# Performance work log

Measured on AMD Instinct MI355X. Metric: run time of the kernel, lower is better.

## Reference

```python
import jax, jax.numpy as jnp
import numpy as np

N = 100000
E = 800000
F_IN = 64
HID = 128


def setup_inputs() -> dict:
    key = jax.random.key(0)
    ks = jax.random.split(key, 10)
    x = jax.random.normal(ks[0], (N, F_IN), dtype=jnp.float32)
    edge_index = jax.random.randint(ks[1], (2, E), 0, N, dtype=jnp.int64)
    s = 0.05
    # PyG GraphConv: lin_rel (with bias) applied to aggregated neighbors, lin_root (no bias) to self
    return {
        "x": x,
        "edge_index": edge_index,
        "W1_rel": jax.random.normal(ks[2], (HID, F_IN), dtype=jnp.float32) * s,
        "b1": jnp.zeros((HID,), dtype=jnp.float32),
        "W1_root": jax.random.normal(ks[3], (HID, F_IN), dtype=jnp.float32) * s,
        "W2_rel": jax.random.normal(ks[4], (HID, HID), dtype=jnp.float32) * s,
        "b2": jnp.zeros((HID,), dtype=jnp.float32),
        "W2_root": jax.random.normal(ks[5], (HID, HID), dtype=jnp.float32) * s,
        "W_fc1": jax.random.normal(ks[6], (20, HID), dtype=jnp.float32) * s,
        "b_fc1": jnp.zeros((20,), dtype=jnp.float32),
        "W_fc2": jax.random.normal(ks[7], (1, 20), dtype=jnp.float32) * s,
        "b_fc2": jnp.zeros((1,), dtype=jnp.float32),
    }


def graph_conv(x, edge_index, W_rel, b_rel, W_root):
    # sum-aggregate source features onto destination nodes (PyG GraphConv, aggr='add')
    src, dst = edge_index[0], edge_index[1]
    agg = jax.ops.segment_sum(x[src], dst, num_segments=N)  # [N, F]
    return agg @ W_rel.T + b_rel + x @ W_root.T


def reference(x, edge_index, W1_rel, b1, W1_root, W2_rel, b2, W2_root,
              W_fc1, b_fc1, W_fc2, b_fc2):
    h = graph_conv(x, edge_index, W1_rel, b1, W1_root)
    h = jax.nn.elu(h)
    h = graph_conv(h, edge_index, W2_rel, b2, W2_root)
    h = jax.nn.relu(h @ W_fc1.T + b_fc1)
    out = h @ W_fc2.T + b_fc2  # [N, 1]
    return out
```

## Files before the change

### kernel.cpp

```cpp
#include <hip/hip_runtime.h>

#define N_NODES 100000
#define N_EDGES 800000
#define FIN 64
#define HID 128
#define NB1 391
#define SRCS_CAP (N_EDGES + 3 * N_NODES)
#define GI (1024 * 256)

typedef unsigned short ushort_t;
typedef __attribute__((ext_vector_type(8))) short short8;
typedef __attribute__((ext_vector_type(16))) float fx16;
typedef __attribute__((ext_vector_type(4))) unsigned short us4;

__device__ inline ushort_t f2bf(float f) {
    unsigned u = __float_as_uint(f);
    u += 0x7fffu + ((u >> 16) & 1u);
    return (ushort_t)(u >> 16);
}

__device__ inline void upadd(float* acc, uint4 A) {
    acc[0] += __uint_as_float(A.x << 16);
    acc[1] += __uint_as_float(A.x & 0xffff0000u);
    acc[2] += __uint_as_float(A.y << 16);
    acc[3] += __uint_as_float(A.y & 0xffff0000u);
    acc[4] += __uint_as_float(A.z << 16);
    acc[5] += __uint_as_float(A.z & 0xffff0000u);
    acc[6] += __uint_as_float(A.w << 16);
    acc[7] += __uint_as_float(A.w & 0xffff0000u);
}

__global__ __launch_bounds__(256) void init_kernel(
    const int* __restrict__ ei, const float* __restrict__ x,
    const float* __restrict__ W1rel, const float* __restrict__ W1root,
    const float* __restrict__ W2rel, const float* __restrict__ W2root,
    const float* __restrict__ b2, const float* __restrict__ Wfc1,
    const float* __restrict__ bfc1, const float* __restrict__ Wfc2,
    int* __restrict__ deg, int* __restrict__ flag, int* __restrict__ srcs,
    ushort_t* __restrict__ xb, ushort_t* __restrict__ Wb1,
    ushort_t* __restrict__ Mb, float* __restrict__ cbp, float* __restrict__ w2p) {
    __shared__ int s[256];
    int t = threadIdx.x;
    int gtid = blockIdx.x * 256 + t;

    if (gtid < N_NODES) deg[gtid] = 0;
    for (int k = gtid; k < SRCS_CAP; k += GI) srcs[k] = N_NODES;
    for (int i = gtid; i < N_NODES * FIN / 4; i += GI) {
        float4 v = ((const float4*)x)[i];
        us4 o = {f2bf(v.x), f2bf(v.y), f2bf(v.z), f2bf(v.w)};
        ((us4*)xb)[i] = o;
    }
    us4 z = {0, 0, 0, 0};
    if (gtid < 16) ((us4*)xb)[(size_t)N_NODES * 16 + gtid] = z;
    if (gtid < HID * HID) {
        int n = gtid >> 7, k = gtid & 127;
        float v = (k < FIN) ? W1rel[n * FIN + k] : W1root[n * FIN + (k - FIN)];
        Wb1[gtid] = f2bf(v);
    }
    if (blockIdx.x < 32) {
        int idx = blockIdx.x * 256 + t;
        int n = idx >> 7, k = idx & 127;
        float acc = 0.f;
        if (n < 20) {
            for (int j = 0; j < HID; j++) acc += Wfc1[n * HID + j] * W2rel[j * HID + k];
        } else if (n >= 32 && n < 52) {
            int m = n - 32;
            for (int j = 0; j < HID; j++) acc += Wfc1[m * HID + j] * W2root[j * HID + k];
        }
        Mb[idx] = f2bf(acc);
    }
    if (blockIdx.x == 32 && t < 32) {
        float cv = 0.f, wv = 0.f;
        if (t < 20) {
            for (int j = 0; j < HID; j++) cv += Wfc1[t * HID + j] * b2[j];
            cv += bfc1[t];
            wv = Wfc2[t];
        }
        cbp[t] = cv;
        w2p[t] = wv;
    }
    if (blockIdx.x == 33) {
        int bad = 0;
        for (int i = t; i < 8192; i += 256) bad |= ei[2 * i + 1];
        s[t] = bad;
        __syncthreads();
        for (int d = 128; d > 0; d >>= 1) {
            if (t < d) s[t] |= s[t + d];
            __syncthreads();
        }
        if (t == 0) *flag = (s[0] != 0) ? 1 : 0;
    }
}

__global__ void hist_kernel(const int* __restrict__ w, const int* __restrict__ flag,
                            int* __restrict__ deg, int* __restrict__ rank) {
    int e = blockIdx.x * 256 + threadIdx.x;
    if (e >= N_EDGES) return;
    int is32 = *flag;
    int d = is32 ? w[N_EDGES + e] : w[2 * (N_EDGES + e)];
    rank[e] = atomicAdd(&deg[d], 1);
}

__global__ void scan1_kernel(const int* __restrict__ deg, int* __restrict__ off,
                             int* __restrict__ bsums) {
    __shared__ int s[256];
    int t = threadIdx.x;
    int i = blockIdx.x * 256 + t;
    int v = (i < N_NODES) ? ((deg[i] + 3) & ~3) : 0;
    s[t] = v;
    __syncthreads();
    for (int d = 1; d < 256; d <<= 1) {
        int w = (t >= d) ? s[t - d] : 0;
        __syncthreads();
        s[t] += w;
        __syncthreads();
    }
    if (i < N_NODES) off[i] = s[t] - v;
    if (t == 255) bsums[blockIdx.x] = s[255];
}

__global__ void scan23_kernel(int* __restrict__ off, const int* __restrict__ bsums) {
    __shared__ int s[256];
    int t = threadIdx.x, b = blockIdx.x;
    int pre = 0, tot = 0;
    for (int j = t; j < NB1; j += 256) {
        int v = bsums[j];
        if (j < b) pre += v;
        tot += v;
    }
    s[t] = pre;
    __syncthreads();
    for (int d = 128; d > 0; d >>= 1) {
        if (t < d) s[t] += s[t + d];
        __syncthreads();
    }
    int prefix = s[0];
    __syncthreads();
    int i = b * 256 + t;
    if (i < N_NODES) off[i] += prefix;
    if (b == 0) {
        s[t] = tot;
        __syncthreads();
        for (int d = 128; d > 0; d >>= 1) {
            if (t < d) s[t] += s[t + d];
            __syncthreads();
        }
        if (t == 0) off[N_NODES] = s[0];
    }
}

__global__ void scatter_kernel(const int* __restrict__ w, const int* __restrict__ flag,
                               const int* __restrict__ off, const int* __restrict__ rank,
                               int* __restrict__ srcs) {
    int e = blockIdx.x * 256 + threadIdx.x;
    if (e >= N_EDGES) return;
    int is32 = *flag;
    int s = is32 ? w[e] : w[2 * e];
    int d = is32 ? w[N_EDGES + e] : w[2 * (N_EDGES + e)];
    srcs[off[d] + rank[e]] = s;
}

__global__ void agg1_kernel(const ushort_t* __restrict__ xb, const int* __restrict__ off,
                            const int* __restrict__ srcs, ushort_t* __restrict__ aggb) {
    int wid = (blockIdx.x * 256 + threadIdx.x) >> 6;
    int lane = threadIdx.x & 63;
    int n = lane >> 3;
    unsigned c = lane & 7;
    int node = wid * 8 + n;
    int b = off[node], e = off[node + 1];
    float acc[8];
#pragma unroll
    for (int j = 0; j < 8; j++) acc[j] = 0.f;
    const uint4* rows = (const uint4*)xb;
    for (int p = b; p < e; p += 4) {
        int4 s = *(const int4*)(srcs + p);
        uint4 A = rows[(unsigned)s.x * 8u + c];
        uint4 B = rows[(unsigned)s.y * 8u + c];
        uint4 C = rows[(unsigned)s.z * 8u + c];
        uint4 D = rows[(unsigned)s.w * 8u + c];
        upadd(acc, A);
        upadd(acc, B);
        upadd(acc, C);
        upadd(acc, D);
    }
    uint4 o = {(unsigned)f2bf(acc[0]) | ((unsigned)f2bf(acc[1]) << 16),
               (unsigned)f2bf(acc[2]) | ((unsigned)f2bf(acc[3]) << 16),
               (unsigned)f2bf(acc[4]) | ((unsigned)f2bf(acc[5]) << 16),
               (unsigned)f2bf(acc[6]) | ((unsigned)f2bf(acc[7]) << 16)};
    ((uint4*)(aggb + (size_t)node * FIN))[c] = o;
}

__global__ __launch_bounds__(256) void g1_kernel(
    const ushort_t* __restrict__ aggb, const ushort_t* __restrict__ xb,
    const ushort_t* __restrict__ Wb1, const float* __restrict__ b1,
    ushort_t* __restrict__ h1b) {
    __shared__ short8 wl8[2048];
    ushort_t* wl = (ushort_t*)wl8;
#pragma unroll
    for (int it = 0; it < 8; it++) {
        int q = it * 256 + threadIdx.x;
        int n = q >> 4, c = q & 15;
        short8 v = ((const short8*)Wb1)[q];
        *(short8*)(wl + n * HID + ((c ^ (n & 7)) << 3)) = v;
    }
    __syncthreads();

    int wave = threadIdx.x >> 6;
    int lane = threadIdx.x & 63;
    int nb = blockIdx.x * 128 + wave * 32;
    if (nb >= N_NODES) return;
    int half = lane >> 5, col = lane & 31;
    int nA = nb + col;
    if (nA >= N_NODES) nA = N_NODES - 1;

    short8 areg[8];
#pragma unroll
    for (int s = 0; s < 4; s++)
        areg[s] = *(const short8*)(aggb + (size_t)nA * FIN + s * 16 + half * 8);
#pragma unroll
    for (int s = 4; s < 8; s++)
        areg[s] = *(const short8*)(xb + (size_t)nA * FIN + (s - 4) * 16 + half * 8);

    fx16 acc[4];
#pragma unroll
    for (int jt = 0; jt < 4; jt++)
#pragma unroll
        for (int r = 0; r < 16; r++) acc[jt][r] = 0.f;

#pragma unroll
    for (int s = 0; s < 8; s++) {
        int c = 2 * s + half;
#pragma unroll
        for (int jt = 0; jt < 4; jt++) {
            int n = jt * 32 + col;
            short8 bq = *(const short8*)(wl + n * HID + ((c ^ (n & 7)) << 3));
            acc[jt] = __builtin_amdgcn_mfma_f32_32x32x16_bf16(areg[s], bq, acc[jt], 0, 0, 0);
        }
    }
#pragma unroll
    for (int jt = 0; jt < 4; jt++) {
        int j = jt * 32 + col;
        float bias = b1[j];
#pragma unroll
        for (int r = 0; r < 16; r++) {
            int node = nb + (r & 3) + 8 * (r >> 2) + 4 * half;
            if (node < N_NODES) {
                float v = acc[jt][r] + bias;
                v = v > 0.f ? v : __expf(v) - 1.f;
                h1b[(size_t)node * HID + j] = f2bf(v);
            }
        }
    }
}

__global__ __launch_bounds__(256) void g2_kernel(
    const ushort_t* __restrict__ h1b, const ushort_t* __restrict__ Mb,
    ushort_t* __restrict__ uvb) {
    __shared__ short8 ml8[1024];
    ushort_t* ml = (ushort_t*)ml8;
    us4 z = {0, 0, 0, 0};
    if (blockIdx.x == 0 && threadIdx.x < 8)
        ((us4*)(uvb + (size_t)N_NODES * 64))[threadIdx.x] = z;
#pragma unroll
    for (int it = 0; it < 4; it++) {
        int q = it * 256 + threadIdx.x;
        int n = q >> 4, c = q & 15;
        short8 v = ((const short8*)Mb)[q];
        *(short8*)(ml + n * HID + ((c ^ (n & 7)) << 3)) = v;
    }
    __syncthreads();

    int wave = threadIdx.x >> 6;
    int lane = threadIdx.x & 63;
    int nb = blockIdx.x * 128 + wave * 32;
    if (nb >= N_NODES) return;
    int half = lane >> 5, col = lane & 31;
    int nA = nb + col;
    if (nA >= N_NODES) nA = N_NODES - 1;

    short8 areg[8];
#pragma unroll
    for (int s = 0; s < 8; s++)
        areg[s] = *(const short8*)(h1b + (size_t)nA * HID + s * 16 + half * 8);

    fx16 acc[2];
#pragma unroll
    for (int jt = 0; jt < 2; jt++)
#pragma unroll
        for (int r = 0; r < 16; r++) acc[jt][r] = 0.f;

#pragma unroll
    for (int s = 0; s < 8; s++) {
        int c = 2 * s + half;
#pragma unroll
        for (int jt = 0; jt < 2; jt++) {
            int n = jt * 32 + col;
            short8 bq = *(const short8*)(ml + n * HID + ((c ^ (n & 7)) << 3));
            acc[jt] = __builtin_amdgcn_mfma_f32_32x32x16_bf16(areg[s], bq, acc[jt], 0, 0, 0);
        }
    }
#pragma unroll
    for (int jt = 0; jt < 2; jt++) {
        int j = jt * 32 + col;
#pragma unroll
        for (int r = 0; r < 16; r++) {
            int node = nb + (r & 3) + 8 * (r >> 2) + 4 * half;
            if (node < N_NODES) uvb[(size_t)node * 64 + j] = f2bf(acc[jt][r]);
        }
    }
}

__global__ void agg3h_kernel(const ushort_t* __restrict__ uvb, const int* __restrict__ off,
                             const int* __restrict__ srcs, const float* __restrict__ cbp,
                             const float* __restrict__ w2p, const float* __restrict__ bfc2,
                             float* __restrict__ out) {
    int wid = (blockIdx.x * 256 + threadIdx.x) >> 6;
    int lane = threadIdx.x & 63;
    int n = lane >> 2;
    unsigned c = lane & 3;
    int node0 = wid * 16 + n;
    int node = (node0 < N_NODES) ? node0 : N_NODES - 1;
    int b = off[node], e = off[node + 1];
    float acc[8];
#pragma unroll
    for (int j = 0; j < 8; j++) acc[j] = 0.f;
    const uint4* rows = (const uint4*)uvb;
    for (int p = b; p < e; p += 4) {
        int4 s = *(const int4*)(srcs + p);
        uint4 A = rows[(unsigned)s.x * 8u + c];
        uint4 B = rows[(unsigned)s.y * 8u + c];
        uint4 C = rows[(unsigned)s.z * 8u + c];
        uint4 D = rows[(unsigned)s.w * 8u + c];
        upadd(acc, A);
        upadd(acc, B);
        upadd(acc, C);
        upadd(acc, D);
    }
    uint4 V = rows[(size_t)node * 8u + 4u + c];
    float vv[8];
    vv[0] = __uint_as_float(V.x << 16);
    vv[1] = __uint_as_float(V.x & 0xffff0000u);
    vv[2] = __uint_as_float(V.y << 16);
    vv[3] = __uint_as_float(V.y & 0xffff0000u);
    vv[4] = __uint_as_float(V.z << 16);
    vv[5] = __uint_as_float(V.z & 0xffff0000u);
    vv[6] = __uint_as_float(V.w << 16);
    vv[7] = __uint_as_float(V.w & 0xffff0000u);
    float4 cba = ((const float4*)cbp)[c * 2];
    float4 cbb = ((const float4*)cbp)[c * 2 + 1];
    float4 w2a = ((const float4*)w2p)[c * 2];
    float4 w2b = ((const float4*)w2p)[c * 2 + 1];
    float s = 0.f, a;
    a = acc[0] + vv[0] + cba.x; s += (a > 0.f ? a : 0.f) * w2a.x;
    a = acc[1] + vv[1] + cba.y; s += (a > 0.f ? a : 0.f) * w2a.y;
    a = acc[2] + vv[2] + cba.z; s += (a > 0.f ? a : 0.f) * w2a.z;
    a = acc[3] + vv[3] + cba.w; s += (a > 0.f ? a : 0.f) * w2a.w;
    a = acc[4] + vv[4] + cbb.x; s += (a > 0.f ? a : 0.f) * w2b.x;
    a = acc[5] + vv[5] + cbb.y; s += (a > 0.f ? a : 0.f) * w2b.y;
    a = acc[6] + vv[6] + cbb.z; s += (a > 0.f ? a : 0.f) * w2b.z;
    a = acc[7] + vv[7] + cbb.w; s += (a > 0.f ? a : 0.f) * w2b.w;
    s += __shfl_xor(s, 1);
    s += __shfl_xor(s, 2);
    if (c == 0 && node0 < N_NODES) out[node0] = s + bfc2[0];
}

extern "C" void kernel_launch(void* const* d_in, const int* in_sizes, int n_in,
                              void* d_out, int out_size, void* d_ws, size_t ws_size,
                              hipStream_t stream) {
    const float* x = (const float*)d_in[0];
    const int* ei = (const int*)d_in[1];
    const float* W1rel = (const float*)d_in[2];
    const float* b1 = (const float*)d_in[3];
    const float* W1root = (const float*)d_in[4];
    const float* W2rel = (const float*)d_in[5];
    const float* b2 = (const float*)d_in[6];
    const float* W2root = (const float*)d_in[7];
    const float* Wfc1 = (const float*)d_in[8];
    const float* bfc1 = (const float*)d_in[9];
    const float* Wfc2 = (const float*)d_in[10];
    const float* bfc2 = (const float*)d_in[11];
    float* out = (float*)d_out;

    char* ws = (char*)d_ws;
    size_t o = 0;
    auto alloc = [&](size_t bytes) {
        char* p = ws + o;
        o += (bytes + 255) & ~(size_t)255;
        return p;
    };
    int* deg = (int*)alloc((size_t)N_NODES * 4);
    int* off = (int*)alloc((size_t)(N_NODES + 1) * 4);
    int* bsums = (int*)alloc(4096);
    int* flag = (int*)alloc(256);
    int* rank = (int*)alloc((size_t)N_EDGES * 4);
    int* srcs = (int*)alloc((size_t)SRCS_CAP * 4);
    ushort_t* xb = (ushort_t*)alloc((size_t)(N_NODES + 1) * FIN * 2);
    ushort_t* agg1b = (ushort_t*)alloc((size_t)N_NODES * FIN * 2);
    ushort_t* h1b = (ushort_t*)alloc((size_t)N_NODES * HID * 2);
    ushort_t* uvb = (ushort_t*)alloc((size_t)(N_NODES + 1) * 64 * 2);
    ushort_t* Wb1 = (ushort_t*)alloc((size_t)HID * HID * 2);
    ushort_t* Mb = (ushort_t*)alloc((size_t)64 * HID * 2);
    float* cbp = (float*)alloc(32 * 4);
    float* w2p = (float*)alloc(32 * 4);

    const int GW = (N_NODES + 127) / 128;
    const int GA1 = N_NODES / 32;
    const int GA3 = 1563;

    init_kernel<<<1024, 256, 0, stream>>>(ei, x, W1rel, W1root, W2rel, W2root,
                                          b2, Wfc1, bfc1, Wfc2,
                                          deg, flag, srcs, xb, Wb1, Mb, cbp, w2p);
    hist_kernel<<<(N_EDGES + 255) / 256, 256, 0, stream>>>(ei, flag, deg, rank);
    scan1_kernel<<<NB1, 256, 0, stream>>>(deg, off, bsums);
    scan23_kernel<<<NB1, 256, 0, stream>>>(off, bsums);
    scatter_kernel<<<(N_EDGES + 255) / 256, 256, 0, stream>>>(ei, flag, off, rank, srcs);
    agg1_kernel<<<GA1, 256, 0, stream>>>(xb, off, srcs, agg1b);
    g1_kernel<<<GW, 256, 0, stream>>>(agg1b, xb, Wb1, b1, h1b);
    g2_kernel<<<GW, 256, 0, stream>>>(h1b, Mb, uvb);
    agg3h_kernel<<<GA3, 256, 0, stream>>>(uvb, off, srcs, cbp, w2p, bfc2, out);
}
```

Baseline: 216.1 us.

## Fuse layer-1 and layer-2 GEMMs via LDS; replace rank array with atomic cursors

The two dense MFMA kernels are merged into one. The ELU-activated hidden tile is written into LDS, reusing the W1 buffer, and fed straight into the second GEMM, so the 25.6 MB h1 round trip through global memory is gone. Separately, the CSR build no longer stores a per-edge rank from the histogram atomics. The scatter kernel instead takes positions with atomicAdd on a per-node cursor seeded by the scan. The scatter order within each node's neighbor list therefore becomes nondeterministic, and the fused kernel needs 48 KB of LDS, which may reduce occupancy.

```diff
diff --git a/kernel.cpp b/kernel.cpp
--- a/kernel.cpp
+++ b/kernel.cpp
@@ -93,12 +93,12 @@
 }
 
 __global__ void hist_kernel(const int* __restrict__ w, const int* __restrict__ flag,
-                            int* __restrict__ deg, int* __restrict__ rank) {
+                            int* __restrict__ deg) {
     int e = blockIdx.x * 256 + threadIdx.x;
     if (e >= N_EDGES) return;
     int is32 = *flag;
     int d = is32 ? w[N_EDGES + e] : w[2 * (N_EDGES + e)];
-    rank[e] = atomicAdd(&deg[d], 1);
+    atomicAdd(&deg[d], 1);
 }
 
 __global__ void scan1_kernel(const int* __restrict__ deg, int* __restrict__ off,
@@ -119,7 +119,8 @@
     if (t == 255) bsums[blockIdx.x] = s[255];
 }
 
-__global__ void scan23_kernel(int* __restrict__ off, const int* __restrict__ bsums) {
+__global__ void scan23_kernel(int* __restrict__ off, const int* __restrict__ bsums,
+                              int* __restrict__ cur) {
     __shared__ int s[256];
     int t = threadIdx.x, b = blockIdx.x;
     int pre = 0, tot = 0;
@@ -137,7 +138,11 @@
     int prefix = s[0];
     __syncthreads();
     int i = b * 256 + t;
-    if (i < N_NODES) off[i] += prefix;
+    if (i < N_NODES) {
+        int v = off[i] + prefix;
+        off[i] = v;
+        cur[i] = v;
+    }
     if (b == 0) {
         s[t] = tot;
         __syncthreads();
@@ -150,14 +155,14 @@
 }
 
 __global__ void scatter_kernel(const int* __restrict__ w, const int* __restrict__ flag,
-                               const int* __restrict__ off, const int* __restrict__ rank,
-                               int* __restrict__ srcs) {
+                               int* __restrict__ cur, int* __restrict__ srcs) {
     int e = blockIdx.x * 256 + threadIdx.x;
     if (e >= N_EDGES) return;
     int is32 = *flag;
     int s = is32 ? w[e] : w[2 * e];
     int d = is32 ? w[N_EDGES + e] : w[2 * (N_EDGES + e)];
-    srcs[off[d] + rank[e]] = s;
+    int pos = atomicAdd(&cur[d], 1);
+    srcs[pos] = s;
 }
 
 __global__ void agg1_kernel(const ushort_t* __restrict__ xb, const int* __restrict__ off,
@@ -190,12 +195,25 @@
     ((uint4*)(aggb + (size_t)node * FIN))[c] = o;
 }
 
-__global__ __launch_bounds__(256) void g1_kernel(
+__global__ __launch_bounds__(256) void g12_kernel(
     const ushort_t* __restrict__ aggb, const ushort_t* __restrict__ xb,
     const ushort_t* __restrict__ Wb1, const float* __restrict__ b1,
-    ushort_t* __restrict__ h1b) {
-    __shared__ short8 wl8[2048];
-    ushort_t* wl = (ushort_t*)wl8;
+    const ushort_t* __restrict__ Mb, ushort_t* __restrict__ uvb) {
+    __shared__ ushort_t smem[24576];
+    ushort_t* wl = smem;
+    ushort_t* ml = smem + 16384;
+
+    us4 z = {0, 0, 0, 0};
+    if (blockIdx.x == 0 && threadIdx.x < 8)
+        ((us4*)(uvb + (size_t)N_NODES * 64))[threadIdx.x] = z;
+
+#pragma unroll
+    for (int it = 0; it < 4; it++) {
+        int q = it * 256 + threadIdx.x;
+        int n = q >> 4, c = q & 15;
+        short8 v = ((const short8*)Mb)[q];
+        *(short8*)(ml + n * HID + ((c ^ (n & 7)) << 3)) = v;
+    }
 #pragma unroll
     for (int it = 0; it < 8; it++) {
         int q = it * 256 + threadIdx.x;
@@ -207,9 +225,8 @@
 
     int wave = threadIdx.x >> 6;
     int lane = threadIdx.x & 63;
+    int half = lane >> 5, col = lane & 31;
     int nb = blockIdx.x * 128 + wave * 32;
-    if (nb >= N_NODES) return;
-    int half = lane >> 5, col = lane & 31;
     int nA = nb + col;
     if (nA >= N_NODES) nA = N_NODES - 1;
 
@@ -237,57 +254,34 @@
             acc[jt] = __builtin_amdgcn_mfma_f32_32x32x16_bf16(areg[s], bq, acc[jt], 0, 0, 0);
         }
     }
+    __syncthreads();
+
 #pragma unroll
     for (int jt = 0; jt < 4; jt++) {
         int j = jt * 32 + col;
         float bias = b1[j];
 #pragma unroll
         for (int r = 0; r < 16; r++) {
-            int node = nb + (r & 3) + 8 * (r >> 2) + 4 * half;
-            if (node < N_NODES) {
-                float v = acc[jt][r] + bias;
-                v = v > 0.f ? v : __expf(v) - 1.f;
-                h1b[(size_t)node * HID + j] = f2bf(v);
-            }
-        }
-    }
-}
-
-__global__ __launch_bounds__(256) void g2_kernel(
-    const ushort_t* __restrict__ h1b, const ushort_t* __restrict__ Mb,
-    ushort_t* __restrict__ uvb) {
-    __shared__ short8 ml8[1024];
-    ushort_t* ml = (ushort_t*)ml8;
-    us4 z = {0, 0, 0, 0};
-    if (blockIdx.x == 0 && threadIdx.x < 8)
-        ((us4*)(uvb + (size_t)N_NODES * 64))[threadIdx.x] = z;
-#pragma unroll
-    for (int it = 0; it < 4; it++) {
-        int q = it * 256 + threadIdx.x;
-        int n = q >> 4, c = q & 15;
-        short8 v = ((const short8*)Mb)[q];
-        *(short8*)(ml + n * HID + ((c ^ (n & 7)) << 3)) = v;
-    }
-    __syncthreads();
-
-    int wave = threadIdx.x >> 6;
-    int lane = threadIdx.x & 63;
-    int nb = blockIdx.x * 128 + wave * 32;
-    if (nb >= N_NODES) return;
-    int half = lane >> 5, col = lane & 31;
-    int nA = nb + col;
-    if (nA >= N_NODES) nA = N_NODES - 1;
-
-    short8 areg[8];
-#pragma unroll
-    for (int s = 0; s < 8; s++)
-        areg[s] = *(const short8*)(h1b + (size_t)nA * HID + s * 16 + half * 8);
-
-    fx16 acc[2];
+            int nl = wave * 32 + (r & 3) + 8 * (r >> 2) + 4 * half;
+            float v = acc[jt][r] + bias;
+            v = v > 0.f ? v : __expf(v) - 1.f;
+            wl[nl * HID + (((j >> 3) ^ (nl & 7)) << 3) + (j & 7)] = f2bf(v);
+        }
+    }
+    __syncthreads();
+
+    int nl2 = wave * 32 + col;
+    short8 af[8];
+#pragma unroll
+    for (int s = 0; s < 8; s++) {
+        int c = 2 * s + half;
+        af[s] = *(const short8*)(wl + nl2 * HID + ((c ^ (nl2 & 7)) << 3));
+    }
+    fx16 uacc[2];
 #pragma unroll
     for (int jt = 0; jt < 2; jt++)
 #pragma unroll
-        for (int r = 0; r < 16; r++) acc[jt][r] = 0.f;
+        for (int r = 0; r < 16; r++) uacc[jt][r] = 0.f;
 
 #pragma unroll
     for (int s = 0; s < 8; s++) {
@@ -296,7 +290,7 @@
         for (int jt = 0; jt < 2; jt++) {
             int n = jt * 32 + col;
             short8 bq = *(const short8*)(ml + n * HID + ((c ^ (n & 7)) << 3));
-            acc[jt] = __builtin_amdgcn_mfma_f32_32x32x16_bf16(areg[s], bq, acc[jt], 0, 0, 0);
+            uacc[jt] = __builtin_amdgcn_mfma_f32_32x32x16_bf16(af[s], bq, uacc[jt], 0, 0, 0);
         }
     }
 #pragma unroll
@@ -305,7 +299,7 @@
 #pragma unroll
         for (int r = 0; r < 16; r++) {
             int node = nb + (r & 3) + 8 * (r >> 2) + 4 * half;
-            if (node < N_NODES) uvb[(size_t)node * 64 + j] = f2bf(acc[jt][r]);
+            if (node < N_NODES) uvb[(size_t)node * 64 + j] = f2bf(uacc[jt][r]);
         }
     }
 }
@@ -392,11 +386,10 @@
     int* off = (int*)alloc((size_t)(N_NODES + 1) * 4);
     int* bsums = (int*)alloc(4096);
     int* flag = (int*)alloc(256);
-    int* rank = (int*)alloc((size_t)N_EDGES * 4);
+    int* cur = (int*)alloc((size_t)N_NODES * 4);
     int* srcs = (int*)alloc((size_t)SRCS_CAP * 4);
     ushort_t* xb = (ushort_t*)alloc((size_t)(N_NODES + 1) * FIN * 2);
     ushort_t* agg1b = (ushort_t*)alloc((size_t)N_NODES * FIN * 2);
-    ushort_t* h1b = (ushort_t*)alloc((size_t)N_NODES * HID * 2);
     ushort_t* uvb = (ushort_t*)alloc((size_t)(N_NODES + 1) * 64 * 2);
     ushort_t* Wb1 = (ushort_t*)alloc((size_t)HID * HID * 2);
     ushort_t* Mb = (ushort_t*)alloc((size_t)64 * HID * 2);
@@ -410,12 +403,11 @@
     init_kernel<<<1024, 256, 0, stream>>>(ei, x, W1rel, W1root, W2rel, W2root,
                                           b2, Wfc1, bfc1, Wfc2,
                                           deg, flag, srcs, xb, Wb1, Mb, cbp, w2p);
-    hist_kernel<<<(N_EDGES + 255) / 256, 256, 0, stream>>>(ei, flag, deg, rank);
+    hist_kernel<<<(N_EDGES + 255) / 256, 256, 0, stream>>>(ei, flag, deg);
     scan1_kernel<<<NB1, 256, 0, stream>>>(deg, off, bsums);
-    scan23_kernel<<<NB1, 256, 0, stream>>>(off, bsums);
-    scatter_kernel<<<(N_EDGES + 255) / 256, 256, 0, stream>>>(ei, flag, off, rank, srcs);
+    scan23_kernel<<<NB1, 256, 0, stream>>>(off, bsums, cur);
+    scatter_kernel<<<(N_EDGES + 255) / 256, 256, 0, stream>>>(ei, flag, cur, srcs);
     agg1_kernel<<<GA1, 256, 0, stream>>>(xb, off, srcs, agg1b);
-    g1_kernel<<<GW, 256, 0, stream>>>(agg1b, xb, Wb1, b1, h1b);
-    g2_kernel<<<GW, 256, 0, stream>>>(h1b, Mb, uvb);
+    g12_kernel<<<GW, 256, 0, stream>>>(agg1b, xb, Wb1, b1, Mb, uvb);
     agg3h_kernel<<<GA3, 256, 0, stream>>>(uvb, off, srcs, cbp, w2p, bfc2, out);
 }
```

After: 241.8 us. 1.12x slower.
